# Kernel optimization log

Hardware: AMD Instinct MI355X
Metric: run time of the kernel (lower is better)

The kernel has to match this reference:

```python
import jax, jax.numpy as jnp
import numpy as np
import math

N_HEAD = 16
N_KV_HEAD = 4
HEAD_DIM = 128
ROTARY_DIM = 128
ROTARY_BASE = 10000
N_CTX = 2048


def _sin_cos(rotary_dim, n_ctx, base):
    pos = np.arange(n_ctx, dtype=np.float32)
    dim = np.arange(rotary_dim // 2, dtype=np.float32)
    freq = base ** (dim / (rotary_dim / 2))
    freq = np.concatenate([freq, freq])  # non-adjacent-pairs layout
    angles = pos[:, None] / freq[None, :]
    return jnp.asarray(np.sin(angles)), jnp.asarray(np.cos(angles))


def _rotate_half(x):
    n = x.shape[-1] // 2
    return jnp.concatenate([-x[..., n:], x[..., :n]], axis=-1)


def setup_inputs() -> dict:
    key = jax.random.key(0)
    ks = jax.random.split(key, 5)
    B, T, C = 2, 2048, 2048
    kv = N_KV_HEAD * HEAD_DIM
    s = 0.02
    return {
        "x": jax.random.normal(ks[0], (B, T, C), jnp.float32),
        "Wq": jax.random.normal(ks[1], (C, C), jnp.float32) * s,
        "Wk": jax.random.normal(ks[2], (kv, C), jnp.float32) * s,
        "Wv": jax.random.normal(ks[3], (kv, C), jnp.float32) * s,
        "Wo": jax.random.normal(ks[4], (C, C), jnp.float32) * s,
    }


def reference(x, Wq, Wk, Wv, Wo):
    B, T, C = x.shape
    q = (x @ Wq.T).reshape(B, T, N_HEAD, HEAD_DIM).transpose(0, 2, 1, 3)    # bhtd
    k = (x @ Wk.T).reshape(B, T, N_KV_HEAD, HEAD_DIM).transpose(0, 2, 1, 3)
    v = (x @ Wv.T).reshape(B, T, N_KV_HEAD, HEAD_DIM).transpose(0, 2, 1, 3)

    sin, cos = _sin_cos(ROTARY_DIM, N_CTX, ROTARY_BASE)
    pos = jnp.arange(T)
    c = cos[pos][None, None, :, :]  # 1,1,T,rot
    s = sin[pos][None, None, :, :]
    q = q * c + _rotate_half(q) * s
    k = k * c + _rotate_half(k) * s

    rep = N_HEAD // N_KV_HEAD
    k = jnp.repeat(k, rep, axis=1)
    v = jnp.repeat(v, rep, axis=1)

    scale = 1.0 / math.sqrt(HEAD_DIM)
    att = jnp.einsum("bhqd,bhkd->bhqk", q, k) * scale
    causal = jnp.tril(jnp.ones((T, T), bool))
    att = jnp.where(causal[None, None], att, -jnp.inf)
    att = jax.nn.softmax(att, axis=-1)
    y = jnp.einsum("bhqk,bhkd->bhqd", att, v)
    y = y.transpose(0, 2, 1, 3).reshape(B, T, C)
    return y @ Wo.T
```

## Files before the change

kernel.cpp:

```cpp
#include <hip/hip_runtime.h>
#include <hip/hip_bf16.h>

typedef float f32x4 __attribute__((ext_vector_type(4)));
typedef float f32x16 __attribute__((ext_vector_type(16)));
typedef short s16x8 __attribute__((ext_vector_type(8)));
typedef short s16x4 __attribute__((ext_vector_type(4)));

__device__ __forceinline__ short f2bf(float f) {
  union { float f; unsigned u; } v; v.f = f;
  unsigned r = v.u + 0x7fffu + ((v.u >> 16) & 1u);
  return (short)(r >> 16);
}
__device__ __forceinline__ float bf2f(short s) {
  union { unsigned u; float f; } v; v.u = ((unsigned)(unsigned short)s) << 16;
  return v.f;
}
__device__ __forceinline__ unsigned cvtpk(float lo, float hi) {
  unsigned r;
  asm("v_cvt_pk_bf16_f32 %0, %1, %2" : "=v"(r) : "v"(lo), "v"(hi));
  return r;
}

__device__ __forceinline__ void gload_lds16(const short* g, short* l) {
  __builtin_amdgcn_global_load_lds(
      (const __attribute__((address_space(1))) void*)g,
      (__attribute__((address_space(3))) void*)l, 16, 0, 0);
}

__global__ __launch_bounds__(256) void k_f2bfw(const float* __restrict__ sx,
                                               const float* __restrict__ s0,
                                               const float* __restrict__ s1,
                                               const float* __restrict__ s2,
                                               const float* __restrict__ s3,
                                               short* __restrict__ dx,
                                               short* __restrict__ dqkv,
                                               short* __restrict__ dwo) {
  int i = blockIdx.x * 256 + threadIdx.x;
  const float* src;
  short* dst;
  if (i < 1048576) { src = sx + (size_t)i * 8; dst = dx + (size_t)i * 8; }
  else if (i < 1572864) { int j = i - 1048576; src = s0 + (size_t)j * 8; dst = dqkv + (size_t)j * 8; }
  else if (i < 1703936) { int j = i - 1572864; src = s1 + (size_t)j * 8; dst = dqkv + 4194304 + (size_t)j * 8; }
  else if (i < 1835008) { int j = i - 1703936; src = s2 + (size_t)j * 8; dst = dqkv + 5242880 + (size_t)j * 8; }
  else { int j = i - 1835008; src = s3 + (size_t)j * 8; dst = dwo + (size_t)j * 8; }
  const float4* p = (const float4*)src;
  float4 a = p[0], b = p[1];
  s16x8 o;
  o[0] = f2bf(a.x); o[1] = f2bf(a.y); o[2] = f2bf(a.z); o[3] = f2bf(a.w);
  o[4] = f2bf(b.x); o[5] = f2bf(b.y); o[6] = f2bf(b.z); o[7] = f2bf(b.w);
  *(s16x8*)dst = o;
}

template <int MODE>
__global__ __launch_bounds__(256) void k_gemm_bt(const short* __restrict__ A,
                                                 const short* __restrict__ Bw,
                                                 void* __restrict__ C,
                                                 void* __restrict__ C2,
                                                 void* __restrict__ C3,
                                                 int M, int N, int K) {
  __shared__ __align__(16) short As[128 * 64];
  __shared__ __align__(16) short Bs[128 * 64];
  const int tid = threadIdx.x;
  const int w = tid >> 6, lane = tid & 63;
  const int wm = w >> 1, wn = w & 1;
  const int nbx = gridDim.x;
  const int f = blockIdx.y * nbx + blockIdx.x;
  const int cpx = (nbx * gridDim.y) >> 3;
  const int sw = (f & 7) * cpx + (f >> 3);
  const int bm = sw / nbx, bn = sw % nbx;
  const int l15 = lane & 15, l4 = lane >> 4;

  f32x4 acc[4][4] = {};

  const int nk = K >> 6;
  for (int kt = 0; kt < nk; ++kt) {
    __syncthreads();
#pragma unroll
    for (int it = 0; it < 4; ++it) {
      int p = it * 256 + tid;
      int p0 = it * 256 + w * 64;
      int r = p >> 3, j = p & 7;
      int jsrc = j ^ (r & 7);
      gload_lds16(A + (size_t)(bm * 128 + r) * K + kt * 64 + jsrc * 8, &As[p0 * 8]);
      gload_lds16(Bw + (size_t)(bn * 128 + r) * K + kt * 64 + jsrc * 8, &Bs[p0 * 8]);
    }
    __syncthreads();
#pragma unroll
    for (int kk = 0; kk < 2; ++kk) {
      s16x8 af[4], bf[4];
      const int jj = kk * 4 + l4;
#pragma unroll
      for (int mi = 0; mi < 4; ++mi) {
        int r = wm * 64 + mi * 16 + l15;
        af[mi] = *(const s16x8*)&As[(r * 8 + (jj ^ (r & 7))) * 8];
      }
#pragma unroll
      for (int ni = 0; ni < 4; ++ni) {
        int r = wn * 64 + ni * 16 + l15;
        bf[ni] = *(const s16x8*)&Bs[(r * 8 + (jj ^ (r & 7))) * 8];
      }
      __builtin_amdgcn_s_setprio(1);
#pragma unroll
      for (int mi = 0; mi < 4; ++mi)
#pragma unroll
        for (int ni = 0; ni < 4; ++ni)
          acc[mi][ni] = __builtin_amdgcn_mfma_f32_16x16x32_bf16(
              af[mi], bf[ni], acc[mi][ni], 0, 0, 0);
      __builtin_amdgcn_s_setprio(0);
    }
  }

#pragma unroll
  for (int mi = 0; mi < 4; ++mi) {
#pragma unroll
    for (int ni = 0; ni < 4; ++ni) {
      int row0 = bm * 128 + wm * 64 + mi * 16 + l4 * 4;
      int col = bn * 128 + wn * 64 + ni * 16 + l15;
      if (MODE == 1) {
        float* Cf = (float*)C;
#pragma unroll
        for (int r2 = 0; r2 < 4; ++r2)
          Cf[(size_t)(row0 + r2) * N + col] = acc[mi][ni][r2];
      } else {
        if (col < 2048) {
          short* Qo = (short*)C;
#pragma unroll
          for (int r2 = 0; r2 < 4; ++r2)
            Qo[(size_t)(row0 + r2) * 2048 + col] = f2bf(acc[mi][ni][r2]);
        } else if (col < 2560) {
          short* Ko = (short*)C2;
#pragma unroll
          for (int r2 = 0; r2 < 4; ++r2)
            Ko[(size_t)(row0 + r2) * 512 + (col - 2048)] = f2bf(acc[mi][ni][r2]);
        } else {
          short* Vo = (short*)C3;
          int b = row0 >> 11, t0 = row0 & 2047;
          s16x4 pk;
#pragma unroll
          for (int r2 = 0; r2 < 4; ++r2) pk[r2] = f2bf(acc[mi][ni][r2]);
          *(s16x4*)&Vo[(size_t)b * 1048576 + (size_t)(col - 2560) * 2048 + t0] = pk;
        }
      }
    }
  }
}

__global__ __launch_bounds__(256) void k_rope(short* __restrict__ X, int shift,
                                              int rowstride, float mul,
                                              int* __restrict__ qcnt) {
  int idx = blockIdx.x * 256 + threadIdx.x;
  if (idx == 0) *qcnt = 0;
  int row = idx >> shift;
  int rem = idx & ((1 << shift) - 1);
  int h = rem >> 6, d = rem & 63;
  int t = row & 2047;
  float inv = exp2f(-(float)d * (13.287712379549449f / 64.f));
  float ang = (float)t * inv;
  float s, c;
  sincosf(ang, &s, &c);
  size_t base = (size_t)row * rowstride + h * 128 + d;
  float q0 = bf2f(X[base]), q1 = bf2f(X[base + 64]);
  X[base] = f2bf((q0 * c - q1 * s) * mul);
  X[base + 64] = f2bf((q1 * c + q0 * s) * mul);
}

__global__ __launch_bounds__(256, 2) void k_attn4(const short* __restrict__ Q,
                                                  const short* __restrict__ Kb,
                                                  const short* __restrict__ Vt,
                                                  short* __restrict__ Y,
                                                  int* __restrict__ qcnt) {
  __shared__ __align__(16) short Ks[2][64 * 128];
  __shared__ __align__(16) short Vs[2][128 * 64];
  __shared__ int s_item;

  const int tid = threadIdx.x;
  const int w = tid >> 6, lane = tid & 63;
  const int l31 = lane & 31, h5 = lane >> 5;
  const int qc0 = (w >> 1) << 5;
  const int par = w & 1;

  float invt[32];
#pragma unroll
  for (int f = 0; f < 4; ++f)
#pragma unroll
    for (int e = 0; e < 8; ++e) {
      int d = f * 16 + h5 * 8 + e;
      invt[f * 8 + e] = exp2f((float)d * (-13.287712379549449f / 64.f));
    }

  for (;;) {
    if (tid == 0) s_item = atomicAdd(qcnt, 1);
    __syncthreads();
    const int item = s_item;
    if (item >= 1024) return;
    const int qi = 31 - (item >> 5);
    const int h = (item >> 1) & 15;
    const int b = item & 1;
    const int kh = h >> 2;
    const int q0 = qi << 6;

    s16x8 qf[8];
    const size_t qrow = (size_t)(b * 2048 + q0 + qc0 + l31);
#pragma unroll
    for (int f = 0; f < 8; ++f)
      qf[f] = *(const s16x8*)(Q + qrow * 2048 + h * 128 + f * 16 + h5 * 8);

    {
      const float tpos = (float)(q0 + qc0 + l31);
#pragma unroll
      for (int f = 0; f < 4; ++f) {
#pragma unroll
        for (int e = 0; e < 8; ++e) {
          float sn, cs;
          __sincosf(tpos * invt[f * 8 + e], &sn, &cs);
          float a = bf2f(qf[f][e]), bv = bf2f(qf[f + 4][e]);
          qf[f][e]     = f2bf((a * cs - bv * sn) * 0.12751758912141852f);
          qf[f + 4][e] = f2bf((bv * cs + a * sn) * 0.12751758912141852f);
        }
      }
    }

    f32x16 oacc[4] = {};
    float m = -1e30f, l = 0.f;

    auto stage = [&](int buf, int t) {
#pragma unroll
      for (int it = 0; it < 4; ++it) {
        int p = it * 256 + tid;
        int p0 = it * 256 + w * 64;
        int r = p >> 4, c = p & 15;
        int csrc = (c - r) & 15;
        gload_lds16(Kb + (size_t)(b * 2048 + t * 64 + r) * 512 + kh * 128 + csrc * 8,
                    &Ks[buf][p0 * 8]);
      }
#pragma unroll
      for (int it = 0; it < 4; ++it) {
        int p = it * 256 + tid;
        int p0 = it * 256 + w * 64;
        int r = p >> 3, c = p & 7;
        int csrc = (c - r) & 7;
        gload_lds16(Vt + (size_t)b * 1048576 + (size_t)(kh * 128 + r) * 2048 +
                        t * 64 + csrc * 8,
                    &Vs[buf][p0 * 8]);
      }
    };

    stage(0, 0);
    __syncthreads();

    for (int t = 0; t <= qi; ++t) {
      const int cur = t & 1;
      if (t < qi) stage(cur ^ 1, t + 1);

      const bool skipw = (t == qi) && (w == 1);
      if (!skipw) {
        f32x16 sa = {};
        const int kr = par * 32 + l31;
        __builtin_amdgcn_s_setprio(1);
#pragma unroll
        for (int f = 0; f < 8; ++f) {
          int c = f * 2 + h5;
          s16x8 kf = *(const s16x8*)&Ks[cur][(kr * 16 + ((c + kr) & 15)) * 8];
          sa = __builtin_amdgcn_mfma_f32_32x32x16_bf16(kf, qf[f], sa, 0, 0, 0);
        }
        __builtin_amdgcn_s_setprio(0);

        if (t == qi && (w == 0 || w == 3)) {
#pragma unroll
          for (int rg = 0; rg < 16; ++rg) {
            int krow = (rg & 3) + 8 * (rg >> 2) + 4 * h5;
            if (krow > l31) sa[rg] = -3.0e38f;
          }
        }

        float mx[16];
#pragma unroll
        for (int i = 0; i < 16; ++i) mx[i] = sa[i];
#pragma unroll
        for (int stp = 8; stp > 0; stp >>= 1)
#pragma unroll
          for (int i = 0; i < stp; ++i) mx[i] = fmaxf(mx[i], mx[i + stp]);
        float pm = fmaxf(mx[0], __shfl_xor(mx[0], 32));

        if (!__all(pm - m <= 8.f)) {
          float mn = fmaxf(m, pm);
          float al = exp2f(m - mn);
          m = mn;
          l *= al;
#pragma unroll
          for (int d = 0; d < 4; ++d)
#pragma unroll
            for (int i = 0; i < 16; ++i) oacc[d][i] *= al;
        }

        float sm[16];
#pragma unroll
        for (int i = 0; i < 16; ++i) {
          float e = exp2f(sa[i] - m);
          sa[i] = e;
          sm[i] = e;
        }
#pragma unroll
        for (int stp = 8; stp > 0; stp >>= 1)
#pragma unroll
          for (int i = 0; i < stp; ++i) sm[i] += sm[i + stp];
        l += sm[0] + __shfl_xor(sm[0], 32);

        unsigned u[8], pu[8];
#pragma unroll
        for (int g = 0; g < 4; ++g) {
          u[2 * g]     = cvtpk(sa[4 * g + 0], sa[4 * g + 1]);
          u[2 * g + 1] = cvtpk(sa[4 * g + 2], sa[4 * g + 3]);
        }
#pragma unroll
        for (int g2 = 0; g2 < 8; ++g2) pu[g2] = __shfl_xor(u[g2], 32);
        s16x8 pb[2];
#pragma unroll
        for (int kk = 0; kk < 2; ++kk) {
          union { unsigned uu[4]; s16x8 v; } cv;
          cv.uu[0] = h5 ? pu[4 * kk + 2] : u[4 * kk];
          cv.uu[1] = h5 ? pu[4 * kk + 3] : u[4 * kk + 1];
          cv.uu[2] = h5 ? u[4 * kk + 2]  : pu[4 * kk];
          cv.uu[3] = h5 ? u[4 * kk + 3]  : pu[4 * kk + 1];
          pb[kk] = cv.v;
        }

        __builtin_amdgcn_s_setprio(1);
#pragma unroll
        for (int dblk = 0; dblk < 4; ++dblk) {
#pragma unroll
          for (int kk = 0; kk < 2; ++kk) {
            int r = dblk * 32 + l31;
            int c = par * 4 + kk * 2 + h5;
            int slot = (c + r) & 7;
            s16x8 vf = *(const s16x8*)&Vs[cur][(r * 8 + slot) * 8];
            oacc[dblk] = __builtin_amdgcn_mfma_f32_32x32x16_bf16(vf, pb[kk],
                                                                 oacc[dblk], 0, 0, 0);
          }
        }
        __builtin_amdgcn_s_setprio(0);
      }

      __syncthreads();
    }

    const int base = (h5 * 32 + l31) * 68;
    if (par) {
      float* mg = (w == 1) ? (float*)&Ks[0][0] : (float*)&Vs[0][0];
#pragma unroll
      for (int d = 0; d < 4; ++d)
#pragma unroll
        for (int rg = 0; rg < 4; ++rg) {
          f32x4 tv;
          tv[0] = oacc[d][rg * 4 + 0];
          tv[1] = oacc[d][rg * 4 + 1];
          tv[2] = oacc[d][rg * 4 + 2];
          tv[3] = oacc[d][rg * 4 + 3];
          *(f32x4*)&mg[base + d * 16 + rg * 4] = tv;
        }
      mg[base + 64] = m;
      mg[base + 65] = l;
    }
    __syncthreads();
    if (!par) {
      const float* mg = (w == 0) ? (const float*)&Ks[0][0] : (const float*)&Vs[0][0];
      float m1 = mg[base + 64], l1 = mg[base + 65];
      float ms = fmaxf(m, m1);
      float a0 = exp2f(m - ms), a1 = exp2f(m1 - ms);
      float li = 1.f / (l * a0 + l1 * a1);
#pragma unroll
      for (int d = 0; d < 4; ++d) {
#pragma unroll
        for (int rg = 0; rg < 4; ++rg) {
          f32x4 po = *(const f32x4*)&mg[base + d * 16 + rg * 4];
          float v0 = (oacc[d][rg * 4 + 0] * a0 + po[0] * a1) * li;
          float v1 = (oacc[d][rg * 4 + 1] * a0 + po[1] * a1) * li;
          float v2 = (oacc[d][rg * 4 + 2] * a0 + po[2] * a1) * li;
          float v3 = (oacc[d][rg * 4 + 3] * a0 + po[3] * a1) * li;
          uint2 st;
          st.x = cvtpk(v0, v1);
          st.y = cvtpk(v2, v3);
          int d0 = d * 32 + 8 * rg + 4 * h5;
          *(uint2*)(Y + qrow * 2048 + h * 128 + d0) = st;
        }
      }
    }
  }
}

extern "C" void kernel_launch(void* const* d_in, const int* in_sizes, int n_in,
                              void* d_out, int out_size, void* d_ws, size_t ws_size,
                              hipStream_t stream) {
  (void)in_sizes; (void)n_in; (void)out_size; (void)ws_size;
  const float* x  = (const float*)d_in[0];
  const float* Wq = (const float*)d_in[1];
  const float* Wk = (const float*)d_in[2];
  const float* Wv = (const float*)d_in[3];
  const float* Wo = (const float*)d_in[4];

  char* ws = (char*)d_ws;
  short* xb    = (short*)(ws);
  short* wqkvb = (short*)(ws + 16777216);
  short* wob   = (short*)(ws + 29360128);
  short* Qb    = (short*)(ws + 37748736);
  short* Kb    = (short*)(ws + 54525952);
  short* Vtb   = (short*)(ws + 58720256);
  short* Yb    = (short*)(ws + 62914560);
  int* qcnt    = (int*)(ws + 29360128 - 64);

  k_f2bfw<<<9216, 256, 0, stream>>>(x, Wq, Wk, Wv, Wo, xb, wqkvb, wob);

  k_gemm_bt<3><<<dim3(24, 32), 256, 0, stream>>>(xb, wqkvb, Qb, Kb, Vtb,
                                                 4096, 3072, 2048);

  k_rope<<<4096, 256, 0, stream>>>(Kb, 8, 512, 1.0f, qcnt);

  k_attn4<<<512, 256, 0, stream>>>(Qb, Kb, Vtb, Yb, qcnt);

  k_gemm_bt<1><<<dim3(16, 32), 256, 0, stream>>>(Yb, wob, d_out, nullptr,
                                                 nullptr, 4096, 2048, 2048);
}
```

Measured before the change: 190.2 us.

## Software-pipeline attention: defer PV MFMA by one tile with triple-buffered V

Restructures the attention loop so each iteration issues the QK^T MFMAs for the current K tile together with the P·V MFMAs for the previous tile. This lets matrix work overlap the softmax exp and shuffle latency. V moves to a triple-buffered LDS ring (80 KB shared in total) so the deferred tile is not overwritten, and a drain step after the loop handles the last tile. The larger LDS footprint may limit occupancy to two blocks per CU, and the code carries an extra P fragment in registers across iterations.

```diff
diff --git a/kernel.cpp b/kernel.cpp
--- a/kernel.cpp
+++ b/kernel.cpp
@@ -164,14 +164,17 @@
   X[base + 64] = f2bf((q1 * c + q0 * s) * mul);
 }
 
-__global__ __launch_bounds__(256, 2) void k_attn4(const short* __restrict__ Q,
+__global__ __launch_bounds__(256, 2) void k_attn9(const short* __restrict__ Q,
                                                   const short* __restrict__ Kb,
                                                   const short* __restrict__ Vt,
                                                   short* __restrict__ Y,
                                                   int* __restrict__ qcnt) {
-  __shared__ __align__(16) short Ks[2][64 * 128];
-  __shared__ __align__(16) short Vs[2][128 * 64];
-  __shared__ int s_item;
+  __shared__ __align__(16) char smem[81920];
+  short* KsB = (short*)smem;
+  short* VsB = (short*)(smem + 32768);
+  float* mg0 = (float*)smem;
+  float* mg1 = (float*)(smem + 32768);
+  int* s_item = (int*)(smem + 81916);
 
   const int tid = threadIdx.x;
   const int w = tid >> 6, lane = tid & 63;
@@ -189,9 +192,9 @@
     }
 
   for (;;) {
-    if (tid == 0) s_item = atomicAdd(qcnt, 1);
-    __syncthreads();
-    const int item = s_item;
+    if (tid == 0) *s_item = atomicAdd(qcnt, 1);
+    __syncthreads();
+    const int item = *s_item;
     if (item >= 1024) return;
     const int qi = 31 - (item >> 5);
     const int h = (item >> 1) & 15;
@@ -222,8 +225,11 @@
 
     f32x16 oacc[4] = {};
     float m = -1e30f, l = 0.f;
-
-    auto stage = [&](int buf, int t) {
+    s16x8 pbP[2];
+
+    auto stage = [&](int kbuf, int vbuf, int t) {
+      short* Kd = KsB + kbuf * 8192;
+      short* Vd = VsB + vbuf * 8192;
 #pragma unroll
       for (int it = 0; it < 4; ++it) {
         int p = it * 256 + tid;
@@ -231,7 +237,7 @@
         int r = p >> 4, c = p & 15;
         int csrc = (c - r) & 15;
         gload_lds16(Kb + (size_t)(b * 2048 + t * 64 + r) * 512 + kh * 128 + csrc * 8,
-                    &Ks[buf][p0 * 8]);
+                    &Kd[p0 * 8]);
       }
 #pragma unroll
       for (int it = 0; it < 4; ++it) {
@@ -241,30 +247,49 @@
         int csrc = (c - r) & 7;
         gload_lds16(Vt + (size_t)b * 1048576 + (size_t)(kh * 128 + r) * 2048 +
                         t * 64 + csrc * 8,
-                    &Vs[buf][p0 * 8]);
+                    &Vd[p0 * 8]);
       }
     };
 
-    stage(0, 0);
+    stage(0, 0, 0);
     __syncthreads();
 
     for (int t = 0; t <= qi; ++t) {
-      const int cur = t & 1;
-      if (t < qi) stage(cur ^ 1, t + 1);
+      if (t < qi) stage((t + 1) & 1, (t + 1) % 3, t + 1);
 
       const bool skipw = (t == qi) && (w == 1);
+      const short* Kcur = KsB + (t & 1) * 8192;
+
+      f32x16 sa = {};
       if (!skipw) {
-        f32x16 sa = {};
         const int kr = par * 32 + l31;
         __builtin_amdgcn_s_setprio(1);
 #pragma unroll
         for (int f = 0; f < 8; ++f) {
           int c = f * 2 + h5;
-          s16x8 kf = *(const s16x8*)&Ks[cur][(kr * 16 + ((c + kr) & 15)) * 8];
+          s16x8 kf = *(const s16x8*)&Kcur[(kr * 16 + ((c + kr) & 15)) * 8];
           sa = __builtin_amdgcn_mfma_f32_32x32x16_bf16(kf, qf[f], sa, 0, 0, 0);
         }
         __builtin_amdgcn_s_setprio(0);
-
+      }
+
+      if (t > 0) {
+        const short* Vprev = VsB + ((t - 1) % 3) * 8192;
+        __builtin_amdgcn_s_setprio(1);
+#pragma unroll
+        for (int dblk = 0; dblk < 4; ++dblk)
+#pragma unroll
+          for (int kk = 0; kk < 2; ++kk) {
+            int r = dblk * 32 + l31;
+            int c = par * 4 + kk * 2 + h5;
+            s16x8 vf = *(const s16x8*)&Vprev[(r * 8 + ((c + r) & 7)) * 8];
+            oacc[dblk] = __builtin_amdgcn_mfma_f32_32x32x16_bf16(
+                vf, pbP[kk], oacc[dblk], 0, 0, 0);
+          }
+        __builtin_amdgcn_s_setprio(0);
+      }
+
+      if (!skipw) {
         if (t == qi && (w == 0 || w == 3)) {
 #pragma unroll
           for (int rg = 0; rg < 16; ++rg) {
@@ -314,7 +339,6 @@
         }
 #pragma unroll
         for (int g2 = 0; g2 < 8; ++g2) pu[g2] = __shfl_xor(u[g2], 32);
-        s16x8 pb[2];
 #pragma unroll
         for (int kk = 0; kk < 2; ++kk) {
           union { unsigned uu[4]; s16x8 v; } cv;
@@ -322,31 +346,33 @@
           cv.uu[1] = h5 ? pu[4 * kk + 3] : u[4 * kk + 1];
           cv.uu[2] = h5 ? u[4 * kk + 2]  : pu[4 * kk];
           cv.uu[3] = h5 ? u[4 * kk + 3]  : pu[4 * kk + 1];
-          pb[kk] = cv.v;
-        }
-
-        __builtin_amdgcn_s_setprio(1);
-#pragma unroll
-        for (int dblk = 0; dblk < 4; ++dblk) {
-#pragma unroll
-          for (int kk = 0; kk < 2; ++kk) {
-            int r = dblk * 32 + l31;
-            int c = par * 4 + kk * 2 + h5;
-            int slot = (c + r) & 7;
-            s16x8 vf = *(const s16x8*)&Vs[cur][(r * 8 + slot) * 8];
-            oacc[dblk] = __builtin_amdgcn_mfma_f32_32x32x16_bf16(vf, pb[kk],
-                                                                 oacc[dblk], 0, 0, 0);
-          }
-        }
-        __builtin_amdgcn_s_setprio(0);
+          pbP[kk] = cv.v;
+        }
       }
 
       __syncthreads();
     }
+
+    if (w != 1) {
+      const short* Vlast = VsB + (qi % 3) * 8192;
+      __builtin_amdgcn_s_setprio(1);
+#pragma unroll
+      for (int dblk = 0; dblk < 4; ++dblk)
+#pragma unroll
+        for (int kk = 0; kk < 2; ++kk) {
+          int r = dblk * 32 + l31;
+          int c = par * 4 + kk * 2 + h5;
+          s16x8 vf = *(const s16x8*)&Vlast[(r * 8 + ((c + r) & 7)) * 8];
+          oacc[dblk] = __builtin_amdgcn_mfma_f32_32x32x16_bf16(
+              vf, pbP[kk], oacc[dblk], 0, 0, 0);
+        }
+      __builtin_amdgcn_s_setprio(0);
+    }
+    __syncthreads();
 
     const int base = (h5 * 32 + l31) * 68;
     if (par) {
-      float* mg = (w == 1) ? (float*)&Ks[0][0] : (float*)&Vs[0][0];
+      float* mg = (w == 1) ? mg0 : mg1;
 #pragma unroll
       for (int d = 0; d < 4; ++d)
 #pragma unroll
@@ -363,7 +389,7 @@
     }
     __syncthreads();
     if (!par) {
-      const float* mg = (w == 0) ? (const float*)&Ks[0][0] : (const float*)&Vs[0][0];
+      const float* mg = (w == 0) ? mg0 : mg1;
       float m1 = mg[base + 64], l1 = mg[base + 65];
       float ms = fmaxf(m, m1);
       float a0 = exp2f(m - ms), a1 = exp2f(m1 - ms);
@@ -415,7 +441,7 @@
 
   k_rope<<<4096, 256, 0, stream>>>(Kb, 8, 512, 1.0f, qcnt);
 
-  k_attn4<<<512, 256, 0, stream>>>(Qb, Kb, Vtb, Yb, qcnt);
+  k_attn9<<<512, 256, 0, stream>>>(Qb, Kb, Vtb, Yb, qcnt);
 
   k_gemm_bt<1><<<dim3(16, 32), 256, 0, stream>>>(Yb, wob, d_out, nullptr,
                                                  nullptr, 4096, 2048, 2048);
```

Result: no change. 191.3 us (+0.6%).
